# Kernel optimization log

Measured on AMD Instinct MI355X. Metric: run time of the kernel, lower is better.

Reference implementation:

```python
import jax, jax.numpy as jnp
import numpy as np

T, B, L = 8192, 8, 1024
HID, H, KV, D = 2048, 16, 8, 128
G = H // KV
EPS = 1e-6
SCALE = 1.0 / float(np.sqrt(D))


def _rms(x, w):
    # RMSNorm over last dim (head_dim), eps=1e-6
    return x * jax.lax.rsqrt(jnp.mean(x * x, axis=-1, keepdims=True) + EPS) * w


def _rot_half(x):
    h = x.shape[-1] // 2
    return jnp.concatenate([-x[..., h:], x[..., :h]], axis=-1)


def setup_inputs() -> dict:
    key = jax.random.key(0)
    ks = jax.random.split(key, 12)
    inp = {}
    inp["packed_sequence"] = jax.random.normal(ks[0], (T, HID), jnp.float32)
    # rotary embeddings: per-sample positions 0..L-1, packed
    pos = jnp.tile(jnp.arange(L), B).astype(jnp.float32)
    inv = 1.0 / (10000.0 ** (jnp.arange(0, D, 2, dtype=jnp.float32) / D))
    fr = pos[:, None] * inv[None, :]
    emb = jnp.concatenate([fr, fr], axis=-1)  # [T, D]
    inp["cos"] = jnp.cos(emb)
    inp["sin"] = jnp.sin(emb)
    # per-sample causal float mask (additive): 0 allowed, -1e9 masked
    tril = jnp.tril(jnp.ones((L, L), bool))
    inp["attention_mask"] = jnp.broadcast_to(
        jnp.where(tril, 0.0, -1e9).astype(jnp.float32)[None], (B, L, L)
    )
    # disjoint und/gen routing indexes covering all T tokens
    inp["und_idx"] = jnp.arange(0, T, 2, dtype=jnp.int32)
    inp["gen_idx"] = jnp.arange(1, T, 2, dtype=jnp.int32)
    s = 0.02

    def lin(k, o, i):
        return jax.random.normal(k, (o, i), jnp.float32) * s

    kk = jax.random.split(ks[1], 8)
    inp["Wq_u"] = lin(kk[0], H * D, HID); inp["bq_u"] = jnp.zeros((H * D,), jnp.float32)
    inp["Wk_u"] = lin(kk[1], KV * D, HID); inp["bk_u"] = jnp.zeros((KV * D,), jnp.float32)
    inp["Wv_u"] = lin(kk[2], KV * D, HID); inp["bv_u"] = jnp.zeros((KV * D,), jnp.float32)
    inp["Wo_u"] = lin(kk[3], HID, H * D)
    inp["Wq_g"] = lin(kk[4], H * D, HID); inp["bq_g"] = jnp.zeros((H * D,), jnp.float32)
    inp["Wk_g"] = lin(kk[5], KV * D, HID); inp["bk_g"] = jnp.zeros((KV * D,), jnp.float32)
    inp["Wv_g"] = lin(kk[6], KV * D, HID); inp["bv_g"] = jnp.zeros((KV * D,), jnp.float32)
    inp["Wo_g"] = lin(kk[7], HID, H * D)
    inp["qn_u"] = jnp.ones((D,), jnp.float32); inp["kn_u"] = jnp.ones((D,), jnp.float32)
    inp["qn_g"] = jnp.ones((D,), jnp.float32); inp["kn_g"] = jnp.ones((D,), jnp.float32)
    return inp


def reference(packed_sequence, cos, sin, attention_mask, und_idx, gen_idx,
              Wq_u, bq_u, Wk_u, bk_u, Wv_u, bv_u, Wo_u,
              Wq_g, bq_g, Wk_g, bk_g, Wv_g, bv_g, Wo_g,
              qn_u, kn_u, qn_g, kn_g):
    x_u = packed_sequence[und_idx]  # [T/2, HID]
    x_g = packed_sequence[gen_idx]

    def route(Wu, bu, Wg, bg, width):
        out = jnp.zeros((T, width), packed_sequence.dtype)
        out = out.at[und_idx].set(x_u @ Wu.T + bu)
        out = out.at[gen_idx].set(x_g @ Wg.T + bg)
        return out

    q = route(Wq_u, bq_u, Wq_g, bq_g, H * D).reshape(T, H, D)
    k = route(Wk_u, bk_u, Wk_g, bk_g, KV * D).reshape(T, KV, D)
    v = route(Wv_u, bv_u, Wv_g, bv_g, KV * D).reshape(T, KV, D)

    # routed per-head QK RMSNorm (separate und/gen weights)
    qn = jnp.zeros_like(q).at[und_idx].set(_rms(q[und_idx], qn_u)).at[gen_idx].set(_rms(q[gen_idx], qn_g))
    kn = jnp.zeros_like(k).at[und_idx].set(_rms(k[und_idx], kn_u)).at[gen_idx].set(_rms(k[gen_idx], kn_g))

    c, s = cos[:, None, :], sin[:, None, :]  # unsqueeze_dim=1
    q = qn * c + _rot_half(qn) * s
    k = kn * c + _rot_half(kn) * s

    # GQA expansion: kv head i -> heads i*G..i*G+G-1
    k = jnp.repeat(k, G, axis=1)  # [T, H, D]
    v = jnp.repeat(v, G, axis=1)

    qb = q.reshape(B, L, H, D)
    kb = k.reshape(B, L, H, D)
    vb = v.reshape(B, L, H, D)

    scores = jnp.einsum('blhd,bmhd->bhlm', qb, kb) * SCALE
    scores = scores + attention_mask[:, None, :, :]
    p = jax.nn.softmax(scores, axis=-1)
    o = jnp.einsum('bhlm,bmhd->blhd', p, vb).reshape(T, H * D)

    out = jnp.zeros((T, HID), packed_sequence.dtype)
    out = out.at[und_idx].set(o[und_idx] @ Wo_u.T)
    out = out.at[gen_idx].set(o[gen_idx] @ Wo_g.T)
    return out
```

## Files before the change

kernel.cpp:

```cpp
#include <hip/hip_runtime.h>
#include <hip/hip_bf16.h>
#include <stdint.h>
#include <math.h>

#define T_TOK 8192
#define HID   2048
#define NH    16
#define NKV   8
#define HD    128
#define LSEQ  1024
#define BATCH 8
#define QKV_N 4096
#define KDIM  2048
#define NT32  64
#define SCALE 0.08838834764831845f

typedef __hip_bfloat16 bf16;
typedef __bf16 bf16x8 __attribute__((ext_vector_type(8)));
typedef float  f32x4  __attribute__((ext_vector_type(4)));

typedef const void __attribute__((address_space(1)))* gas_ptr;
typedef void       __attribute__((address_space(3)))* las_ptr;

__device__ __forceinline__ float b2f(bf16 x) { return __bfloat162float(x); }
__device__ __forceinline__ bf16  f2b(float x) { return __float2bfloat16(x); }
__device__ __forceinline__ unsigned short f2u(float x) {
    union { bf16 b; unsigned short u; } c; c.b = __float2bfloat16(x); return c.u;
}

__device__ __forceinline__ bf16x8 ld16(const void* p) {
    union { uint4 u; bf16x8 v; } c;
    c.u = *reinterpret_cast<const uint4*>(p);
    return c.v;
}

__device__ __forceinline__ void cp16(void* lds, const void* g) {
    __builtin_amdgcn_global_load_lds((gas_ptr)g, (las_ptr)lds, 16, 0, 0);
}

#define DSR(dst, base, imm) \
    asm volatile("ds_read_b128 %0, %1 offset:" #imm : "=v"(dst) : "v"(base))
#define SCHEDB() __builtin_amdgcn_sched_barrier(0)
#define LGKM0()  asm volatile("s_waitcnt lgkmcnt(0)")

#define BARX() do { asm volatile("" ::: "memory"); \
                    __builtin_amdgcn_s_barrier();  \
                    asm volatile("" ::: "memory"); } while (0)

__global__ __launch_bounds__(256) void k_f2b(const float* __restrict__ in,
                                             bf16* __restrict__ out, int n) {
    int i = blockIdx.x * blockDim.x + threadIdx.x;
    int stride = gridDim.x * blockDim.x;
    const float4* in4 = (const float4*)in;
    ushort4* out4 = (ushort4*)out;
    int n4 = n >> 2;
    for (int j = i; j < n4; j += stride) {
        float4 v = in4[j];
        ushort4 o;
        o.x = f2u(v.x); o.y = f2u(v.y); o.z = f2u(v.z); o.w = f2u(v.w);
        out4[j] = o;
    }
}

__global__ __launch_bounds__(256) void k_mod(const int* __restrict__ und,
                                             const int* __restrict__ gen,
                                             int* __restrict__ mod, int n) {
    int i = blockIdx.x * blockDim.x + threadIdx.x;
    if (i < n) { mod[und[i]] = 0; mod[gen[i]] = 1; }
}

template<int EPI>
__global__ __launch_bounds__(512)
void k_gemm8p(const bf16* __restrict__ A,
              const bf16* __restrict__ Bw_u, const bf16* __restrict__ Bw_g,
              const int* __restrict__ und, const int* __restrict__ gen,
              const float* __restrict__ bq_u, const float* __restrict__ bk_u,
              const float* __restrict__ bv_u,
              const float* __restrict__ bq_g, const float* __restrict__ bk_g,
              const float* __restrict__ bv_g,
              bf16* __restrict__ outB, float* __restrict__ outF) {
    extern __shared__ char smem[];

    int modg = blockIdx.y;
    const bf16* Bw = modg ? Bw_g : Bw_u;
    const int* idx = modg ? gen : und;
    const float* bq = modg ? bq_g : bq_u;
    const float* bk = modg ? bk_g : bk_u;
    const float* bv = modg ? bv_g : bv_u;

    int gx = gridDim.x;
    int bid = blockIdx.x;
    int sw = (bid & 7) * (gx >> 3) + (bid >> 3);
    int tn = sw >> 4, tm = sw & 15;

    int tid = threadIdx.x;
    int w = tid >> 6, lane = tid & 63;
    int l16 = lane & 15, l4 = lane >> 4;
    int wm = w >> 2, wn = w & 3;

    int chunk = (lane & 3) ^ ((lane >> 3) & 3);
    const bf16* pS[2][2];
#pragma unroll
    for (int j = 0; j < 2; ++j) {
        int R = (j * 8 + w) * 16 + (lane >> 2);
        pS[0][j] = A + (size_t)idx[tm * 256 + R] * KDIM + chunk * 8;
        pS[1][j] = Bw + (size_t)(tn * 256 + R) * KDIM + chunk * 8;
    }

    auto STAGE = [&](int t, int u) {
        char* base = smem + (t & 3) * 32768 + u * 16384 + w * 1024;
        cp16(base,        pS[u][0] + t * 32);
        cp16(base + 8192, pS[u][1] + t * 32);
    };

    f32x4 acc[8][4];
#pragma unroll
    for (int m = 0; m < 8; ++m)
#pragma unroll
        for (int n = 0; n < 4; ++n) acc[m][n] = {0.f, 0.f, 0.f, 0.f};

    STAGE(0, 0); STAGE(0, 1);
    STAGE(1, 0); STAGE(1, 1);
    STAGE(2, 0); STAGE(2, 1);
    SCHEDB();
    asm volatile("s_waitcnt vmcnt(8)");
    __builtin_amdgcn_s_barrier();

    uint32_t cByte = (uint32_t)((l4 ^ ((l16 >> 1) & 3)) << 4);
    uint32_t aOff = (uint32_t)(wm * 128 + l16) * 64 + cByte;
    uint32_t bOff = 16384u + (uint32_t)(wn * 64 + l16) * 64 + cByte;

#pragma unroll 1
    for (int t = 0; t < NT32; ++t) {
        uint32_t toff = (uint32_t)(t & 3) << 15;
        las_ptr aB = (las_ptr)(smem + toff + aOff);
        las_ptr bB = (las_ptr)(smem + toff + bOff);

        bf16x8 b0, b1, b2, b3, a0, a1, a2, a3;
        DSR(b0, bB, 0);    DSR(b1, bB, 1024);
        DSR(b2, bB, 2048); DSR(b3, bB, 3072);
        DSR(a0, aB, 0);    DSR(a1, aB, 1024);
        DSR(a2, aB, 2048); DSR(a3, aB, 3072);
        if (t + 3 < NT32) STAGE(t + 3, 0);
        SCHEDB();
        __builtin_amdgcn_s_barrier();
        LGKM0();
        SCHEDB();
        __builtin_amdgcn_s_setprio(1);
        acc[0][0] = __builtin_amdgcn_mfma_f32_16x16x32_bf16(a0, b0, acc[0][0], 0, 0, 0);
        acc[0][1] = __builtin_amdgcn_mfma_f32_16x16x32_bf16(a0, b1, acc[0][1], 0, 0, 0);
        acc[0][2] = __builtin_amdgcn_mfma_f32_16x16x32_bf16(a0, b2, acc[0][2], 0, 0, 0);
        acc[0][3] = __builtin_amdgcn_mfma_f32_16x16x32_bf16(a0, b3, acc[0][3], 0, 0, 0);
        acc[1][0] = __builtin_amdgcn_mfma_f32_16x16x32_bf16(a1, b0, acc[1][0], 0, 0, 0);
        acc[1][1] = __builtin_amdgcn_mfma_f32_16x16x32_bf16(a1, b1, acc[1][1], 0, 0, 0);
        acc[1][2] = __builtin_amdgcn_mfma_f32_16x16x32_bf16(a1, b2, acc[1][2], 0, 0, 0);
        acc[1][3] = __builtin_amdgcn_mfma_f32_16x16x32_bf16(a1, b3, acc[1][3], 0, 0, 0);
        acc[2][0] = __builtin_amdgcn_mfma_f32_16x16x32_bf16(a2, b0, acc[2][0], 0, 0, 0);
        acc[2][1] = __builtin_amdgcn_mfma_f32_16x16x32_bf16(a2, b1, acc[2][1], 0, 0, 0);
        acc[2][2] = __builtin_amdgcn_mfma_f32_16x16x32_bf16(a2, b2, acc[2][2], 0, 0, 0);
        acc[2][3] = __builtin_amdgcn_mfma_f32_16x16x32_bf16(a2, b3, acc[2][3], 0, 0, 0);
        acc[3][0] = __builtin_amdgcn_mfma_f32_16x16x32_bf16(a3, b0, acc[3][0], 0, 0, 0);
        acc[3][1] = __builtin_amdgcn_mfma_f32_16x16x32_bf16(a3, b1, acc[3][1], 0, 0, 0);
        acc[3][2] = __builtin_amdgcn_mfma_f32_16x16x32_bf16(a3, b2, acc[3][2], 0, 0, 0);
        acc[3][3] = __builtin_amdgcn_mfma_f32_16x16x32_bf16(a3, b3, acc[3][3], 0, 0, 0);
        __builtin_amdgcn_s_setprio(0);
        SCHEDB();
        __builtin_amdgcn_s_barrier();

        bf16x8 a4, a5, a6, a7;
        DSR(a4, aB, 4096); DSR(a5, aB, 5120);
        DSR(a6, aB, 6144); DSR(a7, aB, 7168);
        if (t + 3 < NT32) {
            STAGE(t + 3, 1);
            SCHEDB();
            asm volatile("s_waitcnt vmcnt(8)");
        } else if (t + 2 < NT32) {
            SCHEDB();
            asm volatile("s_waitcnt vmcnt(4)");
        } else {
            SCHEDB();
            asm volatile("s_waitcnt vmcnt(0)");
        }
        __builtin_amdgcn_s_barrier();
        LGKM0();
        SCHEDB();
        __builtin_amdgcn_s_setprio(1);
        acc[4][0] = __builtin_amdgcn_mfma_f32_16x16x32_bf16(a4, b0, acc[4][0], 0, 0, 0);
        acc[4][1] = __builtin_amdgcn_mfma_f32_16x16x32_bf16(a4, b1, acc[4][1], 0, 0, 0);
        acc[4][2] = __builtin_amdgcn_mfma_f32_16x16x32_bf16(a4, b2, acc[4][2], 0, 0, 0);
        acc[4][3] = __builtin_amdgcn_mfma_f32_16x16x32_bf16(a4, b3, acc[4][3], 0, 0, 0);
        acc[5][0] = __builtin_amdgcn_mfma_f32_16x16x32_bf16(a5, b0, acc[5][0], 0, 0, 0);
        acc[5][1] = __builtin_amdgcn_mfma_f32_16x16x32_bf16(a5, b1, acc[5][1], 0, 0, 0);
        acc[5][2] = __builtin_amdgcn_mfma_f32_16x16x32_bf16(a5, b2, acc[5][2], 0, 0, 0);
        acc[5][3] = __builtin_amdgcn_mfma_f32_16x16x32_bf16(a5, b3, acc[5][3], 0, 0, 0);
        acc[6][0] = __builtin_amdgcn_mfma_f32_16x16x32_bf16(a6, b0, acc[6][0], 0, 0, 0);
        acc[6][1] = __builtin_amdgcn_mfma_f32_16x16x32_bf16(a6, b1, acc[6][1], 0, 0, 0);
        acc[6][2] = __builtin_amdgcn_mfma_f32_16x16x32_bf16(a6, b2, acc[6][2], 0, 0, 0);
        acc[6][3] = __builtin_amdgcn_mfma_f32_16x16x32_bf16(a6, b3, acc[6][3], 0, 0, 0);
        acc[7][0] = __builtin_amdgcn_mfma_f32_16x16x32_bf16(a7, b0, acc[7][0], 0, 0, 0);
        acc[7][1] = __builtin_amdgcn_mfma_f32_16x16x32_bf16(a7, b1, acc[7][1], 0, 0, 0);
        acc[7][2] = __builtin_amdgcn_mfma_f32_16x16x32_bf16(a7, b2, acc[7][2], 0, 0, 0);
        acc[7][3] = __builtin_amdgcn_mfma_f32_16x16x32_bf16(a7, b3, acc[7][3], 0, 0, 0);
        __builtin_amdgcn_s_setprio(0);
        SCHEDB();
        __builtin_amdgcn_s_barrier();
    }

    int rowbase = tm * 256 + wm * 128;
    int colbase = tn * 256 + wn * 64;
#pragma unroll
    for (int m = 0; m < 8; ++m) {
#pragma unroll
        for (int r = 0; r < 4; ++r) {
            int row = rowbase + m * 16 + l4 * 4 + r;
            int token = idx[row];
#pragma unroll
            for (int n = 0; n < 4; ++n) {
                int col = colbase + n * 16 + l16;
                float v = acc[m][n][r];
                if (EPI == 0) {
                    float bias = (col < 2048) ? bq[col]
                               : (col < 3072) ? bk[col - 2048] : bv[col - 3072];
                    outB[(size_t)token * QKV_N + col] = f2b(v + bias);
                } else {
                    outF[(size_t)token * HID + col] = v;
                }
            }
        }
    }
}

__global__ __launch_bounds__(256)
void k_normrope(const bf16* __restrict__ qkv,
                const float* __restrict__ cosT, const float* __restrict__ sinT,
                const int* __restrict__ mod,
                const float* __restrict__ qn_u, const float* __restrict__ qn_g,
                const float* __restrict__ kn_u, const float* __restrict__ kn_g,
                bf16* __restrict__ Qo, bf16* __restrict__ Ko) {
    int t = blockIdx.x;
    int tid = threadIdx.x;
    int w = tid >> 6, lane = tid & 63;
    int m = mod[t];
    int b = t >> 10, pos = t & 1023;
    const bf16* row = qkv + (size_t)t * QKV_N;
    int d0 = 2 * lane, d1 = 2 * lane + 1;
    float c0 = cosT[(size_t)t * HD + d0], c1 = cosT[(size_t)t * HD + d1];
    float s0 = sinT[(size_t)t * HD + d0], s1 = sinT[(size_t)t * HD + d1];
    float sgn = (lane < 32) ? -1.f : 1.f;
    const float* qw = m ? qn_g : qn_u;
    const float* kw = m ? kn_g : kn_u;

    for (int u = w; u < 24; u += 4) {
        float v0 = b2f(row[u * HD + d0]);
        float v1 = b2f(row[u * HD + d1]);
        float ss = v0 * v0 + v1 * v1;
#pragma unroll
        for (int msk = 1; msk < 64; msk <<= 1) ss += __shfl_xor(ss, msk);
        float rs = rsqrtf(ss * (1.0f / HD) + 1e-6f);
        const float* wsc = (u < 16) ? qw : kw;
        float n0 = v0 * rs * wsc[d0], n1 = v1 * rs * wsc[d1];
        float o0 = __shfl_xor(n0, 32), o1 = __shfl_xor(n1, 32);
        float r0 = n0 * c0 + sgn * o0 * s0;
        float r1 = n1 * c1 + sgn * o1 * s1;
        if (u < 16) {
            size_t o = ((size_t)(b * NH + u) * LSEQ + pos) * HD;
            Qo[o + d0] = f2b(r0); Qo[o + d1] = f2b(r1);
        } else {
            size_t o = ((size_t)(b * NKV + (u - 16)) * LSEQ + pos) * HD;
            Ko[o + d0] = f2b(r0); Ko[o + d1] = f2b(r1);
        }
    }
}

__global__ __launch_bounds__(256)
void k_vt(const bf16* __restrict__ qkv, bf16* __restrict__ Vt) {
    __shared__ bf16 lds[64][72];
    int bk = blockIdx.x;
    int b = bk >> 3, kv = bk & 7;
    int pos0 = blockIdx.y * 64;
    int d0 = blockIdx.z * 64;
    int tid = threadIdx.x;

#pragma unroll
    for (int it = 0; it < 2; ++it) {
        int c = tid + it * 256;
        int row = c >> 3, col8 = (c & 7) * 8;
        const bf16* src = qkv + (size_t)(b * LSEQ + pos0 + row) * QKV_N
                        + 3072 + kv * HD + d0 + col8;
        *reinterpret_cast<uint4*>(&lds[row][col8]) = *reinterpret_cast<const uint4*>(src);
    }
    __syncthreads();

#pragma unroll
    for (int it = 0; it < 2; ++it) {
        int c = tid + it * 256;
        int drow = c & 63, pos8 = (c >> 6) * 8;
        union { unsigned short s[8]; uint4 u; } g;
#pragma unroll
        for (int j = 0; j < 8; ++j)
            g.s[j] = *reinterpret_cast<const unsigned short*>(&lds[pos8 + j][drow]);
        bf16* dst = Vt + ((size_t)bk * HD + d0 + drow) * LSEQ + pos0 + pos8;
        *reinterpret_cast<uint4*>(dst) = g.u;
    }
}

__global__ __launch_bounds__(256)
void k_attn(const bf16* __restrict__ Q, const bf16* __restrict__ K,
            const bf16* __restrict__ Vt, bf16* __restrict__ O) {
    int bid = blockIdx.x;
    int p = bid & 3;
    int h = (bid >> 2) & 15;
    int b = bid >> 6;
    int tid = threadIdx.x;
    int w = tid >> 6, lane = tid & 63;
    int l16 = lane & 15, l4 = lane >> 4;
    int j = p * 4 + w;

    const bf16* qhb = Q + (size_t)(b * NH + h) * LSEQ * HD;
    int kv = h >> 1;
    const bf16* kb = K + (size_t)(b * NKV + kv) * LSEQ * HD;
    const bf16* vtb = Vt + (size_t)(b * NKV + kv) * HD * LSEQ;

    __shared__ bf16 Pl[4][32][72];

    f32x4 zero = {0.f, 0.f, 0.f, 0.f};

#pragma unroll 1
    for (int half = 0; half < 2; ++half) {
        int rowblk = half ? (31 - j) : j;
        int q0 = rowblk * 32;
        int kend = q0 + 32;

        bf16x8 qf[2][4];
#pragma unroll
        for (int rf = 0; rf < 2; ++rf)
#pragma unroll
            for (int c = 0; c < 4; ++c)
                qf[rf][c] = ld16(qhb + (size_t)(q0 + rf * 16 + l16) * HD + c * 32 + l4 * 8);

        f32x4 oacc[2][8];
#pragma unroll
        for (int rf = 0; rf < 2; ++rf)
#pragma unroll
            for (int d = 0; d < 8; ++d) oacc[rf][d] = zero;
        float mr[2][4], lr[2][4];
#pragma unroll
        for (int rf = 0; rf < 2; ++rf)
#pragma unroll
            for (int r = 0; r < 4; ++r) { mr[rf][r] = -INFINITY; lr[rf][r] = 0.f; }

        for (int kt = 0; kt < kend; kt += 64) {
            f32x4 s[2][4];
#pragma unroll
            for (int rf = 0; rf < 2; ++rf)
#pragma unroll
                for (int kf = 0; kf < 4; ++kf) s[rf][kf] = zero;
#pragma unroll
            for (int c = 0; c < 4; ++c) {
                bf16x8 kf4[4];
#pragma unroll
                for (int kf = 0; kf < 4; ++kf)
                    kf4[kf] = ld16(kb + (size_t)(kt + kf * 16 + l16) * HD + c * 32 + l4 * 8);
#pragma unroll
                for (int rf = 0; rf < 2; ++rf)
#pragma unroll
                    for (int kf = 0; kf < 4; ++kf)
                        s[rf][kf] = __builtin_amdgcn_mfma_f32_16x16x32_bf16(qf[rf][c], kf4[kf], s[rf][kf], 0, 0, 0);
            }
#pragma unroll
            for (int rf = 0; rf < 2; ++rf) {
#pragma unroll
                for (int r = 0; r < 4; ++r) {
                    int qrow = q0 + rf * 16 + l4 * 4 + r;
                    float sc[4];
                    float rm = -1e30f;
#pragma unroll
                    for (int kf = 0; kf < 4; ++kf) {
                        int key = kt + kf * 16 + l16;
                        sc[kf] = (key <= qrow) ? s[rf][kf][r] * SCALE : -1e30f;
                        rm = fmaxf(rm, sc[kf]);
                    }
#pragma unroll
                    for (int msk = 1; msk < 16; msk <<= 1) rm = fmaxf(rm, __shfl_xor(rm, msk));
                    float mn = fmaxf(mr[rf][r], rm);
                    float corr = __expf(mr[rf][r] - mn);
                    mr[rf][r] = mn;
                    float rsum = 0.f;
#pragma unroll
                    for (int kf = 0; kf < 4; ++kf) {
                        float pv = __expf(sc[kf] - mn);
                        rsum += pv;
                        Pl[w][rf * 16 + l4 * 4 + r][kf * 16 + l16] = f2b(pv);
                    }
#pragma unroll
                    for (int msk = 1; msk < 16; msk <<= 1) rsum += __shfl_xor(rsum, msk);
                    lr[rf][r] = lr[rf][r] * corr + rsum;
#pragma unroll
                    for (int d = 0; d < 8; ++d) oacc[rf][d][r] *= corr;
                }
            }
            bf16x8 pf[2][2];
#pragma unroll
            for (int rf = 0; rf < 2; ++rf)
#pragma unroll
                for (int ks = 0; ks < 2; ++ks)
                    pf[rf][ks] = ld16(&Pl[w][rf * 16 + l16][ks * 32 + l4 * 8]);
#pragma unroll
            for (int dt = 0; dt < 8; ++dt) {
#pragma unroll
                for (int ks = 0; ks < 2; ++ks) {
                    bf16x8 vfr = ld16(vtb + (size_t)(dt * 16 + l16) * LSEQ + kt + ks * 32 + l4 * 8);
#pragma unroll
                    for (int rf = 0; rf < 2; ++rf)
                        oacc[rf][dt] = __builtin_amdgcn_mfma_f32_16x16x32_bf16(pf[rf][ks], vfr, oacc[rf][dt], 0, 0, 0);
                }
            }
        }

#pragma unroll
        for (int rf = 0; rf < 2; ++rf)
#pragma unroll
            for (int r = 0; r < 4; ++r) lr[rf][r] = 1.0f / lr[rf][r];
        int trow = b * LSEQ + q0;
#pragma unroll
        for (int rf = 0; rf < 2; ++rf)
#pragma unroll
            for (int dt = 0; dt < 8; ++dt)
#pragma unroll
                for (int r = 0; r < 4; ++r) {
                    int t = trow + rf * 16 + l4 * 4 + r;
                    O[(size_t)t * HID + h * HD + dt * 16 + l16] = f2b(oacc[rf][dt][r] * lr[rf][r]);
                }
    }
}

extern "C" void kernel_launch(void* const* d_in, const int* in_sizes, int n_in,
                              void* d_out, int out_size, void* d_ws, size_t ws_size,
                              hipStream_t stream) {
    const float* x    = (const float*)d_in[0];
    const float* cosT = (const float*)d_in[1];
    const float* sinT = (const float*)d_in[2];
    const int* und = (const int*)d_in[4];
    const int* gen = (const int*)d_in[5];
    const float* Wq_u = (const float*)d_in[6];
    const float* bq_u = (const float*)d_in[7];
    const float* Wk_u = (const float*)d_in[8];
    const float* bk_u = (const float*)d_in[9];
    const float* Wv_u = (const float*)d_in[10];
    const float* bv_u = (const float*)d_in[11];
    const float* Wo_u = (const float*)d_in[12];
    const float* Wq_g = (const float*)d_in[13];
    const float* bq_g = (const float*)d_in[14];
    const float* Wk_g = (const float*)d_in[15];
    const float* bk_g = (const float*)d_in[16];
    const float* Wv_g = (const float*)d_in[17];
    const float* bv_g = (const float*)d_in[18];
    const float* Wo_g = (const float*)d_in[19];
    const float* qn_u = (const float*)d_in[20];
    const float* kn_u = (const float*)d_in[21];
    const float* qn_g = (const float*)d_in[22];
    const float* kn_g = (const float*)d_in[23];
    float* out = (float*)d_out;

    char* ws = (char*)d_ws;
    size_t off = 0;
    auto alloc = [&](size_t bytes) -> void* {
        void* p = ws + off;
        off += (bytes + 255) & ~(size_t)255;
        return p;
    };
    bf16* xb      = (bf16*)alloc((size_t)T_TOK * HID * 2);
    bf16* Wqkv_u  = (bf16*)alloc((size_t)QKV_N * KDIM * 2);
    bf16* Wqkv_g  = (bf16*)alloc((size_t)QKV_N * KDIM * 2);
    bf16* Wob_u   = (bf16*)alloc((size_t)HID * HID * 2);
    bf16* Wob_g   = (bf16*)alloc((size_t)HID * HID * 2);
    int*  mod     = (int*)alloc((size_t)T_TOK * 4);
    bf16* qkv     = (bf16*)alloc((size_t)T_TOK * QKV_N * 2);
    bf16* Qa      = (bf16*)alloc((size_t)BATCH * NH  * LSEQ * HD * 2);
    bf16* Ka      = (bf16*)alloc((size_t)BATCH * NKV * LSEQ * HD * 2);
    bf16* Vt      = (bf16*)alloc((size_t)BATCH * NKV * HD * LSEQ * 2);
    bf16* Ob      = (bf16*)alloc((size_t)T_TOK * HID * 2);
    (void)ws_size; (void)in_sizes; (void)n_in; (void)out_size;

    (void)hipFuncSetAttribute((const void*)k_gemm8p<0>,
                              hipFuncAttributeMaxDynamicSharedMemorySize, 131072);
    (void)hipFuncSetAttribute((const void*)k_gemm8p<1>,
                              hipFuncAttributeMaxDynamicSharedMemorySize, 131072);

    k_f2b<<<1024, 256, 0, stream>>>(x, xb, T_TOK * HID);
    k_f2b<<<1024, 256, 0, stream>>>(Wq_u, Wqkv_u,               2048 * 2048);
    k_f2b<<<1024, 256, 0, stream>>>(Wk_u, Wqkv_u + 2048 * 2048, 1024 * 2048);
    k_f2b<<<1024, 256, 0, stream>>>(Wv_u, Wqkv_u + 3072 * 2048, 1024 * 2048);
    k_f2b<<<1024, 256, 0, stream>>>(Wq_g, Wqkv_g,               2048 * 2048);
    k_f2b<<<1024, 256, 0, stream>>>(Wk_g, Wqkv_g + 2048 * 2048, 1024 * 2048);
    k_f2b<<<1024, 256, 0, stream>>>(Wv_g, Wqkv_g + 3072 * 2048, 1024 * 2048);
    k_f2b<<<1024, 256, 0, stream>>>(Wo_u, Wob_u, 2048 * 2048);
    k_f2b<<<1024, 256, 0, stream>>>(Wo_g, Wob_g, 2048 * 2048);
    k_mod<<<16, 256, 0, stream>>>(und, gen, mod, T_TOK / 2);

    k_gemm8p<0><<<dim3(16 * 16, 2), 512, 131072, stream>>>(
        xb, Wqkv_u, Wqkv_g, und, gen, bq_u, bk_u, bv_u, bq_g, bk_g, bv_g,
        qkv, nullptr);

    k_normrope<<<T_TOK, 256, 0, stream>>>(qkv, cosT, sinT, mod,
                                          qn_u, qn_g, kn_u, kn_g, Qa, Ka);
    k_vt<<<dim3(BATCH * NKV, LSEQ / 64, HD / 64), 256, 0, stream>>>(qkv, Vt);

    k_attn<<<BATCH * NH * 4, 256, 0, stream>>>(Qa, Ka, Vt, Ob);

    k_gemm8p<1><<<dim3(8 * 16, 2), 512, 131072, stream>>>(
        Ob, Wob_u, Wob_g, und, gen, nullptr, nullptr, nullptr,
        nullptr, nullptr, nullptr, nullptr, out);
}
```

Baseline: 478.9 us.

## Restructure GEMM mainloop to double-buffered LDS with one barrier per tile

Changes the projection GEMM pipeline from a 4-stage LDS ring with two barriers per K-tile to a 2-stage double buffer. Each iteration waits for its tile, does one barrier, issues all 12 LDS reads up front with a partial lgkmcnt wait, and prefetches tile t+2 after the closing barrier. Dynamic shared memory drops from 128 KB to 64 KB, which could allow two blocks per CU and removes one barrier per iteration. The cost is a shallower global prefetch depth, so memory latency may be less well hidden.

```diff
diff --git a/kernel.cpp b/kernel.cpp
--- a/kernel.cpp
+++ b/kernel.cpp
@@ -41,11 +41,7 @@
 #define DSR(dst, base, imm) \
     asm volatile("ds_read_b128 %0, %1 offset:" #imm : "=v"(dst) : "v"(base))
 #define SCHEDB() __builtin_amdgcn_sched_barrier(0)
-#define LGKM0()  asm volatile("s_waitcnt lgkmcnt(0)")
-
-#define BARX() do { asm volatile("" ::: "memory"); \
-                    __builtin_amdgcn_s_barrier();  \
-                    asm volatile("" ::: "memory"); } while (0)
+#define LGKM(n)  asm volatile("s_waitcnt lgkmcnt(" #n ")")
 
 __global__ __launch_bounds__(256) void k_f2b(const float* __restrict__ in,
                                              bf16* __restrict__ out, int n) {
@@ -107,10 +103,12 @@
         pS[1][j] = Bw + (size_t)(tn * 256 + R) * KDIM + chunk * 8;
     }
 
-    auto STAGE = [&](int t, int u) {
-        char* base = smem + (t & 3) * 32768 + u * 16384 + w * 1024;
-        cp16(base,        pS[u][0] + t * 32);
-        cp16(base + 8192, pS[u][1] + t * 32);
+    auto STAGE = [&](int t) {
+        char* base = smem + (t & 1) * 32768 + w * 1024;
+        cp16(base,                 pS[0][0] + t * 32);
+        cp16(base + 8192,          pS[0][1] + t * 32);
+        cp16(base + 16384,         pS[1][0] + t * 32);
+        cp16(base + 16384 + 8192,  pS[1][1] + t * 32);
     };
 
     f32x4 acc[8][4];
@@ -119,12 +117,8 @@
 #pragma unroll
         for (int n = 0; n < 4; ++n) acc[m][n] = {0.f, 0.f, 0.f, 0.f};
 
-    STAGE(0, 0); STAGE(0, 1);
-    STAGE(1, 0); STAGE(1, 1);
-    STAGE(2, 0); STAGE(2, 1);
-    SCHEDB();
-    asm volatile("s_waitcnt vmcnt(8)");
-    __builtin_amdgcn_s_barrier();
+    STAGE(0);
+    STAGE(1);
 
     uint32_t cByte = (uint32_t)((l4 ^ ((l16 >> 1) & 3)) << 4);
     uint32_t aOff = (uint32_t)(wm * 128 + l16) * 64 + cByte;
@@ -132,19 +126,23 @@
 
 #pragma unroll 1
     for (int t = 0; t < NT32; ++t) {
-        uint32_t toff = (uint32_t)(t & 3) << 15;
+        uint32_t toff = (uint32_t)(t & 1) << 15;
         las_ptr aB = (las_ptr)(smem + toff + aOff);
         las_ptr bB = (las_ptr)(smem + toff + bOff);
 
-        bf16x8 b0, b1, b2, b3, a0, a1, a2, a3;
+        SCHEDB();
+        if (t + 1 < NT32) asm volatile("s_waitcnt vmcnt(4)");
+        else              asm volatile("s_waitcnt vmcnt(0)");
+        __builtin_amdgcn_s_barrier();
+
+        bf16x8 b0, b1, b2, b3, a0, a1, a2, a3, a4, a5, a6, a7;
         DSR(b0, bB, 0);    DSR(b1, bB, 1024);
         DSR(b2, bB, 2048); DSR(b3, bB, 3072);
         DSR(a0, aB, 0);    DSR(a1, aB, 1024);
         DSR(a2, aB, 2048); DSR(a3, aB, 3072);
-        if (t + 3 < NT32) STAGE(t + 3, 0);
-        SCHEDB();
-        __builtin_amdgcn_s_barrier();
-        LGKM0();
+        DSR(a4, aB, 4096); DSR(a5, aB, 5120);
+        DSR(a6, aB, 6144); DSR(a7, aB, 7168);
+        LGKM(4);
         SCHEDB();
         __builtin_amdgcn_s_setprio(1);
         acc[0][0] = __builtin_amdgcn_mfma_f32_16x16x32_bf16(a0, b0, acc[0][0], 0, 0, 0);
@@ -165,24 +163,7 @@
         acc[3][3] = __builtin_amdgcn_mfma_f32_16x16x32_bf16(a3, b3, acc[3][3], 0, 0, 0);
         __builtin_amdgcn_s_setprio(0);
         SCHEDB();
-        __builtin_amdgcn_s_barrier();
-
-        bf16x8 a4, a5, a6, a7;
-        DSR(a4, aB, 4096); DSR(a5, aB, 5120);
-        DSR(a6, aB, 6144); DSR(a7, aB, 7168);
-        if (t + 3 < NT32) {
-            STAGE(t + 3, 1);
-            SCHEDB();
-            asm volatile("s_waitcnt vmcnt(8)");
-        } else if (t + 2 < NT32) {
-            SCHEDB();
-            asm volatile("s_waitcnt vmcnt(4)");
-        } else {
-            SCHEDB();
-            asm volatile("s_waitcnt vmcnt(0)");
-        }
-        __builtin_amdgcn_s_barrier();
-        LGKM0();
+        LGKM(0);
         SCHEDB();
         __builtin_amdgcn_s_setprio(1);
         acc[4][0] = __builtin_amdgcn_mfma_f32_16x16x32_bf16(a4, b0, acc[4][0], 0, 0, 0);
@@ -204,6 +185,8 @@
         __builtin_amdgcn_s_setprio(0);
         SCHEDB();
         __builtin_amdgcn_s_barrier();
+        if (t + 2 < NT32) STAGE(t + 2);
+        SCHEDB();
     }
 
     int rowbase = tm * 256 + wm * 128;
@@ -482,11 +465,6 @@
     bf16* Ob      = (bf16*)alloc((size_t)T_TOK * HID * 2);
     (void)ws_size; (void)in_sizes; (void)n_in; (void)out_size;
 
-    (void)hipFuncSetAttribute((const void*)k_gemm8p<0>,
-                              hipFuncAttributeMaxDynamicSharedMemorySize, 131072);
-    (void)hipFuncSetAttribute((const void*)k_gemm8p<1>,
-                              hipFuncAttributeMaxDynamicSharedMemorySize, 131072);
-
     k_f2b<<<1024, 256, 0, stream>>>(x, xb, T_TOK * HID);
     k_f2b<<<1024, 256, 0, stream>>>(Wq_u, Wqkv_u,               2048 * 2048);
     k_f2b<<<1024, 256, 0, stream>>>(Wk_u, Wqkv_u + 2048 * 2048, 1024 * 2048);
@@ -498,7 +476,7 @@
     k_f2b<<<1024, 256, 0, stream>>>(Wo_g, Wob_g, 2048 * 2048);
     k_mod<<<16, 256, 0, stream>>>(und, gen, mod, T_TOK / 2);
 
-    k_gemm8p<0><<<dim3(16 * 16, 2), 512, 131072, stream>>>(
+    k_gemm8p<0><<<dim3(16 * 16, 2), 512, 65536, stream>>>(
         xb, Wqkv_u, Wqkv_g, und, gen, bq_u, bk_u, bv_u, bq_g, bk_g, bv_g,
         qkv, nullptr);
 
@@ -508,7 +486,7 @@
 
     k_attn<<<BATCH * NH * 4, 256, 0, stream>>>(Qa, Ka, Vt, Ob);
 
-    k_gemm8p<1><<<dim3(8 * 16, 2), 512, 131072, stream>>>(
+    k_gemm8p<1><<<dim3(8 * 16, 2), 512, 65536, stream>>>(
         Ob, Wob_u, Wob_g, und, gen, nullptr, nullptr, nullptr,
         nullptr, nullptr, nullptr, nullptr, out);
 }
```

Measured after the change: 486.8 us. No clear change (+1.6%).
